# Kernel optimization log

Measured on AMD Instinct MI355X. Metric: run time of the kernel, lower is better.

The kernel has to match this reference:

```python
import jax, jax.numpy as jnp
import numpy as np

HEADS = 16
HIDDEN = 1024
HEAD_DIM = HIDDEN // HEADS


def setup_inputs() -> dict:
    key = jax.random.key(0)
    ks = jax.random.split(key, 12)
    B, S, H = 2, 2048, HIDDEN
    scale = 1.0 / np.sqrt(H)
    inp = {
        'q': jax.random.normal(ks[0], (B, S, H), jnp.float32),
        'k': jax.random.normal(ks[1], (B, S, H), jnp.float32),
        'v': jax.random.normal(ks[2], (B, S, H), jnp.float32),
        'mask': jnp.ones((B, S), jnp.int32),
        'Wq': jax.random.normal(ks[3], (H, H), jnp.float32) * scale,
        'bq': jnp.zeros((H,), jnp.float32),
        'Wk': jax.random.normal(ks[4], (H, H), jnp.float32) * scale,
        'bk': jnp.zeros((H,), jnp.float32),
        'Wv': jax.random.normal(ks[5], (H, H), jnp.float32) * scale,
        'bv': jnp.zeros((H,), jnp.float32),
        'Wo': jax.random.normal(ks[6], (H, H), jnp.float32) * scale,
        'bo': jnp.zeros((H,), jnp.float32),
    }
    return inp


def reference(q, k, v, mask, Wq, bq, Wk, bk, Wv, bv, Wo, bo):
    B, S, H = q.shape
    hd = HEAD_DIM
    # projections (torch Linear: x @ W.T + b) -> [B, heads, S, hd]
    qh = (q @ Wq.T + bq).reshape(B, S, HEADS, hd).transpose(0, 2, 1, 3)
    kh = (k @ Wk.T + bk).reshape(B, S, HEADS, hd).transpose(0, 2, 1, 3)
    vh = (v @ Wv.T + bv).reshape(B, S, HEADS, hd).transpose(0, 2, 1, 3)
    # full score matrix [B, heads, Sq, Sk]
    scores = jnp.einsum('bhqd,bhkd->bhqk', qh, kh) / np.sqrt(hd)
    # mask [B, Sq] -> [B, 1, Sq, 1], masks entire query rows where mask==0
    m = mask[:, None, :, None]
    scores = jnp.where(m == 0, jnp.float32(-1e9), scores)
    attn = jax.nn.softmax(scores, axis=-1)
    # dropout omitted (eval mode / deterministic)
    y = jnp.einsum('bhqk,bhkd->bhqd', attn, vh)
    y = y.transpose(0, 2, 1, 3).reshape(B, S, H)
    return y @ Wo.T + bo
```

## Files before the change

### kernel.cpp

```cpp
#include <hip/hip_runtime.h>
#include <hip/hip_bf16.h>
#include <cstdint>

#define EL 1048576ull

typedef __bf16 bf16_t;
typedef bf16_t bf16x8 __attribute__((ext_vector_type(8)));
typedef float  f32x4  __attribute__((ext_vector_type(4)));
typedef unsigned int u32x4 __attribute__((ext_vector_type(4)));

__device__ __forceinline__ unsigned short f2bf(float f) {
  unsigned int u = __builtin_bit_cast(unsigned int, f);
  u += 0x7FFFu + ((u >> 16) & 1u);
  return (unsigned short)(u >> 16);
}

__device__ __forceinline__ unsigned int cvtpk(float lo, float hi2) {
  unsigned int r;
  asm("v_cvt_pk_bf16_f32 %0, %1, %2" : "=v"(r) : "v"(lo), "v"(hi2));
  return r;
}

__device__ __forceinline__ float fexp2(float x) {
#if __has_builtin(__builtin_amdgcn_exp2f)
  return __builtin_amdgcn_exp2f(x);
#else
  return exp2f(x);
#endif
}

typedef __attribute__((address_space(1))) void as1_void;
typedef __attribute__((address_space(3))) void as3_void;
__device__ __forceinline__ void load_lds16(const void* g, void* l) {
  __builtin_amdgcn_global_load_lds((as1_void*)g, (as3_void*)l, 16, 0, 0);
}

__device__ __forceinline__ bf16x8 repack_af(const f32x4 s0v, const f32x4 s1v) {
  unsigned int c00 = cvtpk(s0v[0], s0v[1]);
  unsigned int c01 = cvtpk(s0v[2], s0v[3]);
  unsigned int c10 = cvtpk(s1v[0], s1v[1]);
  unsigned int c11 = cvtpk(s1v[2], s1v[3]);
  asm("v_permlane32_swap_b32 %0, %1" : "+v"(c00), "+v"(c10));
  asm("v_permlane16_swap_b32 %0, %1" : "+v"(c00), "+v"(c10));
  asm("v_permlane32_swap_b32 %0, %1" : "+v"(c01), "+v"(c11));
  asm("v_permlane16_swap_b32 %0, %1" : "+v"(c01), "+v"(c11));
  u32x4 wd; wd[0] = c00; wd[1] = c01; wd[2] = c10; wd[3] = c11;
  return __builtin_bit_cast(bf16x8, wd);
}

__global__ __launch_bounds__(256) void convert_all(
    const float* __restrict__ q, const float* __restrict__ k, const float* __restrict__ v,
    const float* __restrict__ wq, const float* __restrict__ wk,
    const float* __restrict__ wv, const float* __restrict__ wo,
    unsigned short* __restrict__ ws)
{
  const size_t total_v4 = 4 * EL;
  for (size_t v4 = (size_t)blockIdx.x * blockDim.x + threadIdx.x; v4 < total_v4;
       v4 += (size_t)gridDim.x * blockDim.x) {
    size_t e = v4 * 4;
    unsigned seg = (unsigned)(e >> 20);
    const float* s; size_t base;
    if      (seg < 4)   { s = q;  base = 0; }
    else if (seg < 8)   { s = k;  base = 4*EL; }
    else if (seg < 12)  { s = v;  base = 8*EL; }
    else if (seg == 12) { s = wq; base = 12*EL; }
    else if (seg == 13) { s = wk; base = 13*EL; }
    else if (seg == 14) { s = wv; base = 14*EL; }
    else                { s = wo; base = 15*EL; }
    const float4 f = *(const float4*)(s + (e - base));
    ushort4 o;
    o.x = f2bf(f.x); o.y = f2bf(f.y); o.z = f2bf(f.z); o.w = f2bf(f.w);
    *(ushort4*)(ws + e) = o;
  }
}

template <int BM, int BN, int WM, int WN, int OUT_BF16>
__device__ __forceinline__ void gemm_bt_core(
    const unsigned short* __restrict__ A,
    const unsigned short* __restrict__ B,
    const float* __restrict__ bias,
    const float scale,
    void* __restrict__ C)
{
  constexpr int K = 1024, N = 1024, BK = 64;
  constexpr int AM = BM / WM / 16, AN = BN / WN / 16;
  __shared__ unsigned short sA[BM * BK];
  __shared__ unsigned short sB[BN * BK];
  const int tid  = threadIdx.x;
  const int wave = tid >> 6, lane = tid & 63;
  const int wm = wave / WN, wn = wave % WN;
  const int tm = blockIdx.y * BM, tn = blockIdx.x * BN;
  const int l16 = lane & 15, hi = lane >> 4, swz = l16 & 7;

  f32x4 acc[AM][AN] = {};

  for (int k0 = 0; k0 < K; k0 += BK) {
    __syncthreads();
#pragma unroll
    for (int i = 0; i < BM * 8 / 256; i++) {
      int p = i * 256 + tid;
      int row = p >> 3, c = p & 7;
      load_lds16(A + (size_t)(tm + row) * K + k0 + ((c ^ (row & 7)) * 8),
                 &sA[(i * 256 + wave * 64) * 8]);
    }
#pragma unroll
    for (int i = 0; i < BN * 8 / 256; i++) {
      int p = i * 256 + tid;
      int row = p >> 3, c = p & 7;
      load_lds16(B + (size_t)(tn + row) * K + k0 + ((c ^ (row & 7)) * 8),
                 &sB[(i * 256 + wave * 64) * 8]);
    }
    __syncthreads();

#pragma unroll
    for (int kk = 0; kk < 2; kk++) {
      bf16x8 af[AM], bfr[AN];
#pragma unroll
      for (int i = 0; i < AM; i++) {
        int row = wm * (BM / WM) + i * 16 + l16;
        af[i] = *(const bf16x8*)&sA[row * BK + (((kk * 4 + hi) ^ swz) * 8)];
      }
#pragma unroll
      for (int j = 0; j < AN; j++) {
        int row = wn * (BN / WN) + j * 16 + l16;
        bfr[j] = *(const bf16x8*)&sB[row * BK + (((kk * 4 + hi) ^ swz) * 8)];
      }
#pragma unroll
      for (int i = 0; i < AM; i++)
#pragma unroll
        for (int j = 0; j < AN; j++)
          acc[i][j] = __builtin_amdgcn_mfma_f32_16x16x32_bf16(af[i], bfr[j], acc[i][j], 0, 0, 0);
    }
  }

#pragma unroll
  for (int i = 0; i < AM; i++) {
    int row0 = tm + wm * (BM / WM) + i * 16 + hi * 4;
#pragma unroll
    for (int j = 0; j < AN; j++) {
      int col = tn + wn * (BN / WN) + j * 16 + l16;
      float bv = bias[col];
#pragma unroll
      for (int r = 0; r < 4; r++) {
        float val = (acc[i][j][r] + bv) * scale;
        if (OUT_BF16) ((unsigned short*)C)[(size_t)(row0 + r) * N + col] = f2bf(val);
        else          ((float*)C)[(size_t)(row0 + r) * N + col] = val;
      }
    }
  }
}

__global__ __launch_bounds__(256, 3) void qkv_gemm(
    const unsigned short* qb, const unsigned short* kb, const unsigned short* vb,
    const unsigned short* wqb, const unsigned short* wkb, const unsigned short* wvb,
    const float* bq, const float* bk, const float* bv,
    unsigned short* Qp, unsigned short* Kp, unsigned short* Vp)
{
  const unsigned short* A; const unsigned short* B; const float* bias; unsigned short* C;
  float scl = 1.0f;
  if (blockIdx.z == 0)      { A = qb; B = wqb; bias = bq; C = Qp; scl = 0.18033688011112042f; }
  else if (blockIdx.z == 1) { A = kb; B = wkb; bias = bk; C = Kp; }
  else                      { A = vb; B = wvb; bias = bv; C = Vp; }
  gemm_bt_core<128, 128, 2, 2, 1>(A, B, bias, scl, C);
}

__global__ __launch_bounds__(256, 2) void out_gemm(
    const unsigned short* Yb, const unsigned short* wob, const float* bo, float* out)
{
  gemm_bt_core<128, 64, 4, 1, 0>(Yb, wob, bo, 1.0f, out);
}

__global__ __launch_bounds__(256) void vt_kernel(
    const unsigned short* __restrict__ Vp, unsigned short* __restrict__ Vt)
{
  __shared__ unsigned short tl[64 * 128];
  const int tid = threadIdx.x;
  const int s0 = blockIdx.x * 128;
  const int bh = blockIdx.y, b = bh >> 4, h = bh & 15;
  const unsigned short* src = Vp + ((size_t)b * 2048 + s0) * 1024 + h * 64;
#pragma unroll
  for (int i = 0; i < 4; i++) {
    int g = i * 256 + tid;
    int s = (g & 63) | ((g >> 9) << 6);
    int c = (g >> 6) & 7;
    u32x4 u = *(const u32x4*)(src + (size_t)s * 1024 + c * 8);
#pragma unroll
    for (int e = 0; e < 8; e++)
      tl[(c * 8 + e) * 128 + s] = (unsigned short)(u[e >> 1] >> ((e & 1) * 16));
  }
  __syncthreads();
  unsigned short* dst = Vt + (size_t)bh * 64 * 2048 + s0;
#pragma unroll
  for (int i = 0; i < 4; i++) {
    int g = i * 256 + tid;
    int d = g >> 4, sc = g & 15;
    *(u32x4*)(dst + (size_t)d * 2048 + sc * 8) = *(const u32x4*)&tl[d * 128 + sc * 8];
  }
}

__global__ __launch_bounds__(512, 4) void attn_kernel(
    const unsigned short* __restrict__ Qp, const unsigned short* __restrict__ Kp,
    const unsigned short* __restrict__ Vt, const int* __restrict__ mask,
    unsigned short* __restrict__ Yb)
{
  constexpr int S = 2048, H = 1024;
  __shared__ unsigned short sK[2][128 * 64];
  __shared__ unsigned short sV[2][64 * 128];

  const int tid = threadIdx.x, wave = tid >> 6, lane = tid & 63;
  const int l16 = lane & 15, hi = lane >> 4, swz = l16 & 7;
  const int qt = blockIdx.x * 256;
  const int h = blockIdx.y, b = blockIdx.z, bh = b * 16 + h;
  const unsigned short* Qb = Qp + (size_t)b * S * H + (size_t)h * 64;
  const unsigned short* Kb = Kp + (size_t)b * S * H + (size_t)h * 64;
  const unsigned short* Vb = Vt + (size_t)bh * 64 * 2048;

  unsigned short* sQ = &sK[0][0];
#pragma unroll
  for (int i = 0; i < 4; i++) {
    int p = i * 512 + tid, row = p >> 3, c = p & 7;
    load_lds16(Qb + (size_t)(qt + row) * H + ((c ^ (row & 7)) * 8),
               &sQ[(i * 512 + wave * 64) * 8]);
  }
  asm volatile("s_waitcnt vmcnt(0)" ::: "memory");
  __builtin_amdgcn_sched_barrier(0);
  __builtin_amdgcn_s_barrier();

  bf16x8 qf[2][2];
#pragma unroll
  for (int m = 0; m < 2; m++) {
    const int row = wave * 32 + m * 16 + l16;
    const int qm = mask[(size_t)b * S + qt + row];
#pragma unroll
    for (int ks = 0; ks < 2; ks++) {
      bf16x8 v = *(const bf16x8*)&sQ[row * 64 + (((ks * 4 + hi) ^ swz) * 8)];
      u32x4 u = __builtin_bit_cast(u32x4, v);
#pragma unroll
      for (int c = 0; c < 4; c++) u[c] = qm ? u[c] : 0u;
      qf[m][ks] = __builtin_bit_cast(bf16x8, u);
    }
  }
  __syncthreads();

#pragma unroll
  for (int i = 0; i < 2; i++) {
    int p = i * 512 + tid, row = p >> 3, c = p & 7;
    load_lds16(Kb + (size_t)row * H + ((c ^ (row & 7)) * 8),
               &sK[0][(i * 512 + wave * 64) * 8]);
  }
#pragma unroll
  for (int i = 0; i < 2; i++) {
    int p = i * 512 + tid, d = p >> 4, kvc = p & 15;
    int sg = ((kvc ^ d) & 7) | (kvc & 8);
    load_lds16(Vb + (size_t)d * 2048 + sg * 8,
               &sV[0][(i * 512 + wave * 64) * 8]);
  }

  float lsum[2] = {0.f, 0.f};
  f32x4 oacc[2][4] = {};

  for (int t = 0; t < 16; t++) {
    const int cur = t & 1;
    if (t < 15) {
      const size_t kv0 = (size_t)(t + 1) * 128;
#pragma unroll
      for (int i = 0; i < 2; i++) {
        int p = i * 512 + tid, row = p >> 3, c = p & 7;
        load_lds16(Kb + (kv0 + row) * H + ((c ^ (row & 7)) * 8),
                   &sK[cur ^ 1][(i * 512 + wave * 64) * 8]);
      }
#pragma unroll
      for (int i = 0; i < 2; i++) {
        int p = i * 512 + tid, d = p >> 4, kvc = p & 15;
        int sg = ((kvc ^ d) & 7) | (kvc & 8);
        load_lds16(Vb + (size_t)d * 2048 + kv0 + sg * 8,
                   &sV[cur ^ 1][(i * 512 + wave * 64) * 8]);
      }
      asm volatile("s_waitcnt vmcnt(4)" ::: "memory");
    } else {
      asm volatile("s_waitcnt vmcnt(0)" ::: "memory");
    }
    __builtin_amdgcn_sched_barrier(0);
    __builtin_amdgcn_s_barrier();

    const unsigned short* kb = sK[cur];
    const unsigned short* vb = sV[cur];

#pragma unroll
    for (int hf = 0; hf < 2; hf++) {
      f32x4 sf[2][4];
#pragma unroll
      for (int jj = 0; jj < 4; jj++) {
        int row = (hf * 4 + jj) * 16 + l16;
        bf16x8 kf0 = *(const bf16x8*)&kb[row * 64 + ((hi ^ swz) * 8)];
        bf16x8 kf1 = *(const bf16x8*)&kb[row * 64 + (((4 + hi) ^ swz) * 8)];
#pragma unroll
        for (int m = 0; m < 2; m++) {
          f32x4 acc = {};
          acc = __builtin_amdgcn_mfma_f32_16x16x32_bf16(kf0, qf[m][0], acc, 0, 0, 0);
          acc = __builtin_amdgcn_mfma_f32_16x16x32_bf16(kf1, qf[m][1], acc, 0, 0, 0);
          sf[m][jj] = acc;
        }
      }

#pragma unroll
      for (int m = 0; m < 2; m++) {
#pragma unroll
        for (int jj = 0; jj < 4; jj++)
#pragma unroll
          for (int r = 0; r < 4; r++)
            sf[m][jj][r] = fexp2(sf[m][jj][r] - 16.0f);
        f32x4 c4 = (sf[m][0] + sf[m][1]) + (sf[m][2] + sf[m][3]);
        lsum[m] += (c4[0] + c4[1]) + (c4[2] + c4[3]);
      }

#pragma unroll
      for (int w2 = 0; w2 < 2; w2++) {
        bf16x8 af0 = repack_af(sf[0][2 * w2], sf[0][2 * w2 + 1]);
        bf16x8 af1 = repack_af(sf[1][2 * w2], sf[1][2 * w2 + 1]);
        const int gw = hf * 2 + w2;
#pragma unroll
        for (int n = 0; n < 4; n++) {
          int d = n * 16 + l16;
          bf16x8 vf = *(const bf16x8*)&vb[d * 128 + (((gw * 4 + hi) ^ swz) * 8)];
          oacc[0][n] = __builtin_amdgcn_mfma_f32_16x16x32_bf16(af0, vf, oacc[0][n], 0, 0, 0);
          oacc[1][n] = __builtin_amdgcn_mfma_f32_16x16x32_bf16(af1, vf, oacc[1][n], 0, 0, 0);
        }
      }
    }
    __builtin_amdgcn_sched_barrier(0);
    __builtin_amdgcn_s_barrier();
  }

#pragma unroll
  for (int m = 0; m < 2; m++) {
    lsum[m] += __shfl_xor(lsum[m], 16);
    lsum[m] += __shfl_xor(lsum[m], 32);
  }
#pragma unroll
  for (int m = 0; m < 2; m++) {
    float lr[4];
#pragma unroll
    for (int r = 0; r < 4; r++) lr[r] = 1.0f / __shfl(lsum[m], hi * 4 + r);
#pragma unroll
    for (int n = 0; n < 4; n++)
#pragma unroll
      for (int r = 0; r < 4; r++) {
        int row = qt + wave * 32 + m * 16 + hi * 4 + r;
        int col = n * 16 + l16;
        Yb[((size_t)b * S + row) * H + h * 64 + col] = f2bf(oacc[m][n][r] * lr[r]);
      }
  }
}

extern "C" void kernel_launch(void* const* d_in, const int* in_sizes, int n_in,
                              void* d_out, int out_size, void* d_ws, size_t ws_size,
                              hipStream_t stream)
{
  const float* q  = (const float*)d_in[0];
  const float* k  = (const float*)d_in[1];
  const float* v  = (const float*)d_in[2];
  const int*  mask = (const int*)d_in[3];
  const float* Wq = (const float*)d_in[4];
  const float* bq = (const float*)d_in[5];
  const float* Wk = (const float*)d_in[6];
  const float* bk = (const float*)d_in[7];
  const float* Wv = (const float*)d_in[8];
  const float* bv = (const float*)d_in[9];
  const float* Wo = (const float*)d_in[10];
  const float* bo = (const float*)d_in[11];

  unsigned short* ws  = (unsigned short*)d_ws;
  unsigned short* qb  = ws;
  unsigned short* kb  = ws + 4 * EL;
  unsigned short* vb  = ws + 8 * EL;
  unsigned short* wqb = ws + 12 * EL;
  unsigned short* wkb = ws + 13 * EL;
  unsigned short* wvb = ws + 14 * EL;
  unsigned short* wob = ws + 15 * EL;
  unsigned short* Qp  = ws + 16 * EL;
  unsigned short* Kp  = ws + 20 * EL;
  unsigned short* Vp  = ws + 24 * EL;
  unsigned short* Yb  = ws + 28 * EL;
  unsigned short* VtG = ws;

  convert_all<<<2048, 256, 0, stream>>>(q, k, v, Wq, Wk, Wv, Wo, ws);
  qkv_gemm<<<dim3(8, 32, 3), 256, 0, stream>>>(qb, kb, vb, wqb, wkb, wvb,
                                               bq, bk, bv, Qp, Kp, Vp);
  vt_kernel<<<dim3(16, 32), 256, 0, stream>>>(Vp, VtG);
  attn_kernel<<<dim3(8, 16, 2), 512, 0, stream>>>(Qp, Kp, VtG, mask, Yb);
  out_gemm<<<dim3(16, 32), 256, 0, stream>>>(Yb, wob, bo, (float*)d_out);
}
```

Measured before the change: 128.5 us.

## Fuse V transpose into QKV GEMM epilogue and raise MFMA wave priority

The V projection epilogue now writes its output directly in the per-head transposed layout the attention kernel reads, so the separate transpose kernel and its extra read and write pass over V are gone. The attention kernel also wraps its MFMA sections in s_setprio so matrix-issuing waves are favoured over waves doing exp and repack work. The transposed stores are 8-byte writes strided by 2048 elements, which coalesce less well than the original row-major stores.

```diff
diff --git a/kernel.cpp b/kernel.cpp
--- a/kernel.cpp
+++ b/kernel.cpp
@@ -7,6 +7,7 @@
 typedef __bf16 bf16_t;
 typedef bf16_t bf16x8 __attribute__((ext_vector_type(8)));
 typedef float  f32x4  __attribute__((ext_vector_type(4)));
+typedef unsigned int u32x2 __attribute__((ext_vector_type(2)));
 typedef unsigned int u32x4 __attribute__((ext_vector_type(4)));
 
 __device__ __forceinline__ unsigned short f2bf(float f) {
@@ -74,15 +75,13 @@
   }
 }
 
-template <int BM, int BN, int WM, int WN, int OUT_BF16>
-__device__ __forceinline__ void gemm_bt_core(
+template <int BM, int BN, int WM, int WN>
+__device__ __forceinline__ void gemm_bt_main(
     const unsigned short* __restrict__ A,
     const unsigned short* __restrict__ B,
-    const float* __restrict__ bias,
-    const float scale,
-    void* __restrict__ C)
-{
-  constexpr int K = 1024, N = 1024, BK = 64;
+    f32x4 (&acc)[BM / WM / 16][BN / WN / 16])
+{
+  constexpr int K = 1024, BK = 64;
   constexpr int AM = BM / WM / 16, AN = BN / WN / 16;
   __shared__ unsigned short sA[BM * BK];
   __shared__ unsigned short sB[BN * BK];
@@ -92,8 +91,6 @@
   const int tm = blockIdx.y * BM, tn = blockIdx.x * BN;
   const int l16 = lane & 15, hi = lane >> 4, swz = l16 & 7;
 
-  f32x4 acc[AM][AN] = {};
-
   for (int k0 = 0; k0 < K; k0 += BK) {
     __syncthreads();
 #pragma unroll
@@ -132,69 +129,81 @@
           acc[i][j] = __builtin_amdgcn_mfma_f32_16x16x32_bf16(af[i], bfr[j], acc[i][j], 0, 0, 0);
     }
   }
-
-#pragma unroll
-  for (int i = 0; i < AM; i++) {
-    int row0 = tm + wm * (BM / WM) + i * 16 + hi * 4;
-#pragma unroll
-    for (int j = 0; j < AN; j++) {
-      int col = tn + wn * (BN / WN) + j * 16 + l16;
-      float bv = bias[col];
-#pragma unroll
-      for (int r = 0; r < 4; r++) {
-        float val = (acc[i][j][r] + bv) * scale;
-        if (OUT_BF16) ((unsigned short*)C)[(size_t)(row0 + r) * N + col] = f2bf(val);
-        else          ((float*)C)[(size_t)(row0 + r) * N + col] = val;
-      }
-    }
-  }
 }
 
 __global__ __launch_bounds__(256, 3) void qkv_gemm(
     const unsigned short* qb, const unsigned short* kb, const unsigned short* vb,
     const unsigned short* wqb, const unsigned short* wkb, const unsigned short* wvb,
     const float* bq, const float* bk, const float* bv,
-    unsigned short* Qp, unsigned short* Kp, unsigned short* Vp)
-{
-  const unsigned short* A; const unsigned short* B; const float* bias; unsigned short* C;
-  float scl = 1.0f;
-  if (blockIdx.z == 0)      { A = qb; B = wqb; bias = bq; C = Qp; scl = 0.18033688011112042f; }
-  else if (blockIdx.z == 1) { A = kb; B = wkb; bias = bk; C = Kp; }
-  else                      { A = vb; B = wvb; bias = bv; C = Vp; }
-  gemm_bt_core<128, 128, 2, 2, 1>(A, B, bias, scl, C);
+    unsigned short* Qp, unsigned short* Kp, unsigned short* Vt)
+{
+  const unsigned short* A; const unsigned short* B; const float* bias;
+  if (blockIdx.z == 0)      { A = qb; B = wqb; bias = bq; }
+  else if (blockIdx.z == 1) { A = kb; B = wkb; bias = bk; }
+  else                      { A = vb; B = wvb; bias = bv; }
+
+  f32x4 acc[4][4] = {};
+  gemm_bt_main<128, 128, 2, 2>(A, B, acc);
+
+  const int tid = threadIdx.x, wave = tid >> 6, lane = tid & 63;
+  const int wm = wave >> 1, wn = wave & 1;
+  const int tm = blockIdx.y * 128, tn = blockIdx.x * 128;
+  const int l16 = lane & 15, hi = lane >> 4;
+
+  if (blockIdx.z < 2) {
+    unsigned short* C = (blockIdx.z == 0) ? Qp : Kp;
+    const float scale = (blockIdx.z == 0) ? 0.18033688011112042f : 1.0f;
+#pragma unroll
+    for (int i = 0; i < 4; i++) {
+      int row0 = tm + wm * 64 + i * 16 + hi * 4;
+#pragma unroll
+      for (int j = 0; j < 4; j++) {
+        int col = tn + wn * 64 + j * 16 + l16;
+        float bv2 = bias[col];
+#pragma unroll
+        for (int r = 0; r < 4; r++)
+          C[(size_t)(row0 + r) * 1024 + col] = f2bf((acc[i][j][r] + bv2) * scale);
+      }
+    }
+  } else {
+#pragma unroll
+    for (int i = 0; i < 4; i++) {
+      int row0 = tm + wm * 64 + i * 16 + hi * 4;
+      int bb = row0 >> 11, s = row0 & 2047;
+#pragma unroll
+      for (int j = 0; j < 4; j++) {
+        int col = tn + wn * 64 + j * 16 + l16;
+        int hh = col >> 6, d = col & 63;
+        float bv2 = bias[col];
+        u32x2 w;
+        w[0] = cvtpk(acc[i][j][0] + bv2, acc[i][j][1] + bv2);
+        w[1] = cvtpk(acc[i][j][2] + bv2, acc[i][j][3] + bv2);
+        *(u32x2*)&Vt[((size_t)(bb * 16 + hh) * 64 + d) * 2048 + s] = w;
+      }
+    }
+  }
 }
 
 __global__ __launch_bounds__(256, 2) void out_gemm(
     const unsigned short* Yb, const unsigned short* wob, const float* bo, float* out)
 {
-  gemm_bt_core<128, 64, 4, 1, 0>(Yb, wob, bo, 1.0f, out);
-}
-
-__global__ __launch_bounds__(256) void vt_kernel(
-    const unsigned short* __restrict__ Vp, unsigned short* __restrict__ Vt)
-{
-  __shared__ unsigned short tl[64 * 128];
-  const int tid = threadIdx.x;
-  const int s0 = blockIdx.x * 128;
-  const int bh = blockIdx.y, b = bh >> 4, h = bh & 15;
-  const unsigned short* src = Vp + ((size_t)b * 2048 + s0) * 1024 + h * 64;
-#pragma unroll
-  for (int i = 0; i < 4; i++) {
-    int g = i * 256 + tid;
-    int s = (g & 63) | ((g >> 9) << 6);
-    int c = (g >> 6) & 7;
-    u32x4 u = *(const u32x4*)(src + (size_t)s * 1024 + c * 8);
-#pragma unroll
-    for (int e = 0; e < 8; e++)
-      tl[(c * 8 + e) * 128 + s] = (unsigned short)(u[e >> 1] >> ((e & 1) * 16));
-  }
-  __syncthreads();
-  unsigned short* dst = Vt + (size_t)bh * 64 * 2048 + s0;
-#pragma unroll
-  for (int i = 0; i < 4; i++) {
-    int g = i * 256 + tid;
-    int d = g >> 4, sc = g & 15;
-    *(u32x4*)(dst + (size_t)d * 2048 + sc * 8) = *(const u32x4*)&tl[d * 128 + sc * 8];
+  f32x4 acc[2][4] = {};
+  gemm_bt_main<128, 64, 4, 1>(Yb, wob, acc);
+
+  const int tid = threadIdx.x, wave = tid >> 6, lane = tid & 63;
+  const int tm = blockIdx.y * 128, tn = blockIdx.x * 64;
+  const int l16 = lane & 15, hi = lane >> 4;
+#pragma unroll
+  for (int i = 0; i < 2; i++) {
+    int row0 = tm + wave * 32 + i * 16 + hi * 4;
+#pragma unroll
+    for (int j = 0; j < 4; j++) {
+      int col = tn + j * 16 + l16;
+      float bv2 = bo[col];
+#pragma unroll
+      for (int r = 0; r < 4; r++)
+        out[(size_t)(row0 + r) * 1024 + col] = acc[i][j][r] + bv2;
+    }
   }
 }
 
@@ -289,6 +298,7 @@
 #pragma unroll
     for (int hf = 0; hf < 2; hf++) {
       f32x4 sf[2][4];
+      __builtin_amdgcn_s_setprio(1);
 #pragma unroll
       for (int jj = 0; jj < 4; jj++) {
         int row = (hf * 4 + jj) * 16 + l16;
@@ -302,6 +312,7 @@
           sf[m][jj] = acc;
         }
       }
+      __builtin_amdgcn_s_setprio(0);
 
 #pragma unroll
       for (int m = 0; m < 2; m++) {
@@ -319,6 +330,7 @@
         bf16x8 af0 = repack_af(sf[0][2 * w2], sf[0][2 * w2 + 1]);
         bf16x8 af1 = repack_af(sf[1][2 * w2], sf[1][2 * w2 + 1]);
         const int gw = hf * 2 + w2;
+        __builtin_amdgcn_s_setprio(1);
 #pragma unroll
         for (int n = 0; n < 4; n++) {
           int d = n * 16 + l16;
@@ -326,6 +338,7 @@
           oacc[0][n] = __builtin_amdgcn_mfma_f32_16x16x32_bf16(af0, vf, oacc[0][n], 0, 0, 0);
           oacc[1][n] = __builtin_amdgcn_mfma_f32_16x16x32_bf16(af1, vf, oacc[1][n], 0, 0, 0);
         }
+        __builtin_amdgcn_s_setprio(0);
       }
     }
     __builtin_amdgcn_sched_barrier(0);
@@ -380,14 +393,12 @@
   unsigned short* wob = ws + 15 * EL;
   unsigned short* Qp  = ws + 16 * EL;
   unsigned short* Kp  = ws + 20 * EL;
-  unsigned short* Vp  = ws + 24 * EL;
+  unsigned short* Vt  = ws + 24 * EL;
   unsigned short* Yb  = ws + 28 * EL;
-  unsigned short* VtG = ws;
 
   convert_all<<<2048, 256, 0, stream>>>(q, k, v, Wq, Wk, Wv, Wo, ws);
   qkv_gemm<<<dim3(8, 32, 3), 256, 0, stream>>>(qb, kb, vb, wqb, wkb, wvb,
-                                               bq, bk, bv, Qp, Kp, Vp);
-  vt_kernel<<<dim3(16, 32), 256, 0, stream>>>(Vp, VtG);
-  attn_kernel<<<dim3(8, 16, 2), 512, 0, stream>>>(Qp, Kp, VtG, mask, Yb);
+                                               bq, bk, bv, Qp, Kp, Vt);
+  attn_kernel<<<dim3(8, 16, 2), 512, 0, stream>>>(Qp, Kp, Vt, mask, Yb);
   out_gemm<<<dim3(16, 32), 256, 0, stream>>>(Yb, wob, bo, (float*)d_out);
 }
```

Result: faster. 124.8 us (-2.9%).
